# Optimization experiments

Hardware: AMD Instinct MI355X
Metric: run time of the kernel (lower is better)

## Reference

```python
import jax, jax.numpy as jnp
import numpy as np

B, N, D_IN, D_OUT = 512, 64, 2048, 1024
EPS = 1e-12  # layer_norm_epsilon


def setup_inputs() -> dict:
    key = jax.random.key(0)
    k0, k1, k2, k3, k4 = jax.random.split(key, 5)
    img_feats = jax.random.normal(k0, (B, N, D_IN), jnp.float32)
    boxes = jax.random.normal(k1, (B, N, 7), jnp.float32)
    box_mask = jax.random.randint(k2, (B, N), 0, 2, jnp.int32)
    obj_labels = jax.random.randint(k3, (B, N), 0, 91, jnp.int32)
    # Learned params: obj_downsample Linear(2048->1024), LayerNorm(1024)
    W = jax.random.normal(k4, (D_IN, D_OUT), jnp.float32) * 0.02
    b = jnp.zeros((D_OUT,), jnp.float32)
    ln_w = jnp.ones((D_OUT,), jnp.float32)
    ln_b = jnp.zeros((D_OUT,), jnp.float32)
    return {"img_feats": img_feats, "boxes": boxes, "box_mask": box_mask,
            "obj_labels": obj_labels, "W": W, "b": b, "ln_w": ln_w, "ln_b": ln_b}


def reference(img_feats, boxes, box_mask, obj_labels, W, b, ln_w, ln_b):
    # Dropout(p=0.1) is identity in eval mode.
    # Linear + ReLU applied to every (padded) box; per-row ops so padded rows
    # are computed then masked — same math as gathering valid rows first.
    h = jax.nn.relu(jnp.einsum('bnd,df->bnf', img_feats, W) + b)  # [B,N,1024]
    mu = jnp.mean(h, axis=-1, keepdims=True)
    var = jnp.mean(jnp.square(h - mu), axis=-1, keepdims=True)
    ln = (h - mu) * jax.lax.rsqrt(var + EPS) * ln_w + ln_b  # LayerNorm
    # pad_sequence repack: left-align each image's valid boxes (stable sort
    # keeps original order among valid boxes), zero the padded tail.
    order = jnp.argsort(1 - box_mask, axis=1, stable=True)  # valid first
    packed = jnp.take_along_axis(ln, order[:, :, None], axis=1)
    m = jnp.take_along_axis(box_mask, order, axis=1).astype(ln.dtype)
    return packed * m[:, :, None]  # obj_reps: [B, N, 1024]
```

## Files before the change

### kernel.cpp

```cpp
#include <hip/hip_runtime.h>
#include <hip/hip_bf16.h>

typedef __attribute__((ext_vector_type(8))) short short8;
typedef __attribute__((ext_vector_type(4))) short short4v;
typedef __attribute__((ext_vector_type(4))) float f32x4;

#define D_IN   2048
#define D_OUT  1024

__device__ __forceinline__ short f2bf(float x) {
    union { __hip_bfloat16 h; short s; } u;
    u.h = __float2bfloat16(x);
    return u.s;
}

__global__ void transpose_w_kernel(const float* __restrict__ W,
                                   short* __restrict__ Bt) {
    __shared__ float tile[32][33];
    int c0 = blockIdx.x * 32;
    int r0 = blockIdx.y * 32;
    int tc = threadIdx.x & 31;
    int tr = threadIdx.x >> 5;
#pragma unroll
    for (int i = 0; i < 32; i += 8)
        tile[tr + i][tc] = W[(long)(r0 + tr + i) * D_OUT + c0 + tc];
    __syncthreads();
#pragma unroll
    for (int i = 0; i < 32; i += 8)
        Bt[(long)(c0 + tr + i) * D_IN + r0 + tc] = f2bf(tile[tc][tr + i]);
}


#define BAR()    __builtin_amdgcn_s_barrier()
#define SB0()    __builtin_amdgcn_sched_barrier(0)
#define LGKM0()  do { asm volatile("s_waitcnt lgkmcnt(0)" ::: "memory"); SB0(); } while (0)
#define VMW(n)   do { asm volatile("s_waitcnt vmcnt(" #n ")" ::: "memory"); SB0(); } while (0)

__global__ __launch_bounds__(512, 2)
void fused_kernel(const float* __restrict__ img, const short* __restrict__ Bt,
                  const float* __restrict__ bias, const int* __restrict__ mask,
                  const float* __restrict__ lnw, const float* __restrict__ lnb,
                  float* __restrict__ out) {
    __shared__ char LDS[139264];
#define LDSB(buf) (LDS + (buf) * 65536)
#define LDSA(buf) (LDS + 131072 + (buf) * 4096)

    const int b    = blockIdx.x;
    const int tid  = threadIdx.x;
    const int lane = tid & 63;
    const int w    = tid >> 6;
    const int lrow = lane & 15;
    const int lchk = lane >> 4;

    const int  bsw   = (tid & 3) ^ ((tid >> 2) & 3) ^ ((tid >> 4) & 3);
    const short* bsrc0 = Bt + (long)(tid >> 2) * D_IN + bsw * 8;
    const long arowg = (long)b * 64 + (tid >> 3);
    const int  ak4   = (tid & 7) * 4;
    const int  arl    = tid >> 3;
    const int  achk   = (tid & 7) >> 1;
    const int  awoff  = (arl * 4 + (achk ^ (arl & 3) ^ ((arl >> 2) & 3))) * 16 + (tid & 1) * 8;
    const int  fsw = ((lchk ^ (lrow & 3) ^ ((lrow >> 2) & 3)) << 4);
    const int  afb = lrow * 64 + fsw;
    const int  bfb = w * 8192 + lrow * 64 + fsw;

#define B_GLD(buf, k0) do {                                                         \
    _Pragma("unroll") for (int i = 0; i < 8; ++i)                                   \
        __builtin_amdgcn_global_load_lds(                                           \
            (const __attribute__((address_space(1))) void*)(bsrc0 + (long)i * 128 * D_IN + (k0)), \
            (__attribute__((address_space(3))) void*)(LDSB(buf) + i * 8192 + tid * 16), 16, 0, 0); \
} while (0)
#define A_LOAD(k0)  do { stA = *(const float4*)(img + arowg * D_IN + (k0) + ak4); } while (0)
#define A_WRITE(buf) do {                                                           \
    short4v c_; c_[0] = f2bf(stA.x); c_[1] = f2bf(stA.y);                           \
    c_[2] = f2bf(stA.z); c_[3] = f2bf(stA.w);                                       \
    *(short4v*)(LDSA(buf) + awoff) = c_;                                            \
} while (0)
#define FRAG_READ(fa, fb, abuf, bbuf) do {                                          \
    _Pragma("unroll") for (int mi = 0; mi < 4; ++mi)                                \
        fa[mi] = *(const short8*)((abuf) + afb + mi * 1024);                        \
    _Pragma("unroll") for (int nf = 0; nf < 8; ++nf)                                \
        fb[nf] = *(const short8*)((bbuf) + bfb + nf * 1024);                        \
} while (0)
#define MFMA_T(fa, fb) do {                                                         \
    __builtin_amdgcn_s_setprio(1);                                                  \
    _Pragma("unroll") for (int mi = 0; mi < 4; ++mi)                                \
    _Pragma("unroll") for (int nf = 0; nf < 8; ++nf)                                \
        acc[mi][nf] = __builtin_amdgcn_mfma_f32_16x16x32_bf16(                      \
            fa[mi], fb[nf], acc[mi][nf], 0, 0, 0);                                  \
    __builtin_amdgcn_s_setprio(0);                                                  \
} while (0)
#define TILE(faP, fbP, faN, fbN, parbuf, npbuf, t) do {                             \
    VMW(0);                                    \
    A_WRITE(npbuf);                                              \
    LGKM0(); BAR(); SB0();                 \
    { int k2_ = (((t) + 2) & 63) * 32; A_LOAD(k2_); B_GLD(parbuf, k2_); }           \
    FRAG_READ(faN, fbN, LDSA(npbuf), LDSB(npbuf));                                  \
    MFMA_T(faP, fbP);                                                               \
} while (0)

    f32x4 acc[4][8];
#pragma unroll
    for (int i = 0; i < 4; ++i)
#pragma unroll
        for (int j = 0; j < 8; ++j) acc[i][j] = (f32x4)0.0f;

    float4 stA;
    short8 fA0[4], fB0[8], fA1[4], fB1[8];

    A_LOAD(0);
    B_GLD(0, 0);
    VMW(8);
    A_WRITE(0);
    A_LOAD(32);
    B_GLD(1, 32);
    VMW(9);
    LGKM0(); BAR(); SB0();
    FRAG_READ(fA0, fB0, LDSA(0), LDSB(0));

#pragma unroll 1
    for (int t = 0; t < 64; t += 2) {
        TILE(fA0, fB0, fA1, fB1, 0, 1, t);
        TILE(fA1, fB1, fA0, fB0, 1, 0, t + 1);
    }

    VMW(0); LGKM0(); BAR(); SB0();

    float* redS = (float*)LDS;
    float* redQ = (float*)(LDS + 2048);
    float* muT  = (float*)(LDS + 4096);
    float* rsT  = (float*)(LDS + 4352);

    float bb[8];
#pragma unroll
    for (int nf = 0; nf < 8; ++nf) bb[nf] = bias[w * 128 + nf * 16 + lrow];

    float s[4][4], q[4][4];
#pragma unroll
    for (int mi = 0; mi < 4; ++mi)
#pragma unroll
        for (int r = 0; r < 4; ++r) { s[mi][r] = 0.f; q[mi][r] = 0.f; }
#pragma unroll
    for (int mi = 0; mi < 4; ++mi)
#pragma unroll
        for (int nf = 0; nf < 8; ++nf)
#pragma unroll
            for (int r = 0; r < 4; ++r) {
                float v = fmaxf(acc[mi][nf][r] + bb[nf], 0.f);
                acc[mi][nf][r] = v;
                s[mi][r] += v;
                q[mi][r] += v * v;
            }
#pragma unroll
    for (int mi = 0; mi < 4; ++mi)
#pragma unroll
        for (int r = 0; r < 4; ++r)
#pragma unroll
            for (int off = 1; off <= 8; off <<= 1) {
                s[mi][r] += __shfl_xor(s[mi][r], off);
                q[mi][r] += __shfl_xor(q[mi][r], off);
            }
    if (lrow == 0) {
#pragma unroll
        for (int mi = 0; mi < 4; ++mi)
#pragma unroll
            for (int r = 0; r < 4; ++r) {
                int m = mi * 16 + lchk * 4 + r;
                redS[w * 64 + m] = s[mi][r];
                redQ[w * 64 + m] = q[mi][r];
            }
    }
    LGKM0(); BAR(); SB0();
    if (tid < 64) {
        float S = 0.f, Q = 0.f;
#pragma unroll
        for (int ww = 0; ww < 8; ++ww) { S += redS[ww * 64 + tid]; Q += redQ[ww * 64 + tid]; }
        float mu  = S * (1.0f / 1024.0f);
        float var = Q * (1.0f / 1024.0f) - mu * mu;
        muT[tid] = mu;
        rsT[tid] = rsqrtf(var + 1e-12f);
    }
    LGKM0(); BAR(); SB0();

    int mv = mask[(b << 6) | lane];
    unsigned long long bal = __ballot(mv != 0);
    int cnt = __popcll(bal);

    float lw[8], lb[8];
#pragma unroll
    for (int nf = 0; nf < 8; ++nf) {
        int col = w * 128 + nf * 16 + lrow;
        lw[nf] = lnw[col];
        lb[nf] = lnb[col];
    }
#pragma unroll
    for (int mi = 0; mi < 4; ++mi)
#pragma unroll
        for (int r = 0; r < 4; ++r) {
            int m = mi * 16 + lchk * 4 + r;
            if ((bal >> m) & 1ull) {
                int d = __popcll(bal & ((1ull << m) - 1ull));
                float mu = muT[m], rs = rsT[m];
                long obase = ((long)(b << 6) + d) * D_OUT + w * 128 + lrow;
#pragma unroll
                for (int nf = 0; nf < 8; ++nf)
                    out[obase + nf * 16] = (acc[mi][nf][r] - mu) * rs * lw[nf] + lb[nf];
            }
        }
    for (int d = cnt; d < 64; ++d) {
        float2 z = make_float2(0.f, 0.f);
        *(float2*)(out + ((long)(b << 6) + d) * D_OUT + w * 128 + lane * 2) = z;
    }
}

extern "C" void kernel_launch(void* const* d_in, const int* in_sizes, int n_in,
                              void* d_out, int out_size, void* d_ws, size_t ws_size,
                              hipStream_t stream) {
    const float* img  = (const float*)d_in[0];
    const int*   mask = (const int*)d_in[2];
    const float* W    = (const float*)d_in[4];
    const float* bias = (const float*)d_in[5];
    const float* lnw  = (const float*)d_in[6];
    const float* lnb  = (const float*)d_in[7];
    float* out = (float*)d_out;

    short* Bt = (short*)d_ws;

    transpose_w_kernel<<<dim3(D_OUT / 32, D_IN / 32), 256, 0, stream>>>(W, Bt);
    fused_kernel<<<512, 512, 0, stream>>>(img, Bt, bias, mask, lnw, lnb, out);
}
```

Before: 282.8 us.

## Replace double-buffered direct-to-LDS pipeline with single-buffer register-staged loads

Drops the two-stage LDS double buffer fed by global_load_lds and stages both the A and B tiles through registers, writing them into a single LDS buffer each iteration. This halves LDS use, from about 136KB to 68KB. Two barriers per k-step now separate the writes from the fragment reads, and the fragment reads no longer overlap the previous tile's MFMAs. The intent is simpler scheduling and possibly more resident blocks, at the cost of more VGPRs for the staged B data and less overlap between loads and compute.

```diff
diff --git a/kernel.cpp b/kernel.cpp
--- a/kernel.cpp
+++ b/kernel.cpp
@@ -34,16 +34,13 @@
 #define BAR()    __builtin_amdgcn_s_barrier()
 #define SB0()    __builtin_amdgcn_sched_barrier(0)
 #define LGKM0()  do { asm volatile("s_waitcnt lgkmcnt(0)" ::: "memory"); SB0(); } while (0)
-#define VMW(n)   do { asm volatile("s_waitcnt vmcnt(" #n ")" ::: "memory"); SB0(); } while (0)
 
 __global__ __launch_bounds__(512, 2)
 void fused_kernel(const float* __restrict__ img, const short* __restrict__ Bt,
                   const float* __restrict__ bias, const int* __restrict__ mask,
                   const float* __restrict__ lnw, const float* __restrict__ lnb,
                   float* __restrict__ out) {
-    __shared__ char LDS[139264];
-#define LDSB(buf) (LDS + (buf) * 65536)
-#define LDSA(buf) (LDS + 131072 + (buf) * 4096)
+    __shared__ char LDS[69632];
 
     const int b    = blockIdx.x;
     const int tid  = threadIdx.x;
@@ -52,51 +49,20 @@
     const int lrow = lane & 15;
     const int lchk = lane >> 4;
 
-    const int  bsw   = (tid & 3) ^ ((tid >> 2) & 3) ^ ((tid >> 4) & 3);
-    const short* bsrc0 = Bt + (long)(tid >> 2) * D_IN + bsw * 8;
-    const long arowg = (long)b * 64 + (tid >> 3);
-    const int  ak4   = (tid & 7) * 4;
-    const int  arl    = tid >> 3;
-    const int  achk   = (tid & 7) >> 1;
-    const int  awoff  = (arl * 4 + (achk ^ (arl & 3) ^ ((arl >> 2) & 3))) * 16 + (tid & 1) * 8;
-    const int  fsw = ((lchk ^ (lrow & 3) ^ ((lrow >> 2) & 3)) << 4);
-    const int  afb = lrow * 64 + fsw;
-    const int  bfb = w * 8192 + lrow * 64 + fsw;
-
-#define B_GLD(buf, k0) do {                                                         \
-    _Pragma("unroll") for (int i = 0; i < 8; ++i)                                   \
-        __builtin_amdgcn_global_load_lds(                                           \
-            (const __attribute__((address_space(1))) void*)(bsrc0 + (long)i * 128 * D_IN + (k0)), \
-            (__attribute__((address_space(3))) void*)(LDSB(buf) + i * 8192 + tid * 16), 16, 0, 0); \
-} while (0)
-#define A_LOAD(k0)  do { stA = *(const float4*)(img + arowg * D_IN + (k0) + ak4); } while (0)
-#define A_WRITE(buf) do {                                                           \
-    short4v c_; c_[0] = f2bf(stA.x); c_[1] = f2bf(stA.y);                           \
-    c_[2] = f2bf(stA.z); c_[3] = f2bf(stA.w);                                       \
-    *(short4v*)(LDSA(buf) + awoff) = c_;                                            \
-} while (0)
-#define FRAG_READ(fa, fb, abuf, bbuf) do {                                          \
-    _Pragma("unroll") for (int mi = 0; mi < 4; ++mi)                                \
-        fa[mi] = *(const short8*)((abuf) + afb + mi * 1024);                        \
-    _Pragma("unroll") for (int nf = 0; nf < 8; ++nf)                                \
-        fb[nf] = *(const short8*)((bbuf) + bfb + nf * 1024);                        \
-} while (0)
-#define MFMA_T(fa, fb) do {                                                         \
-    __builtin_amdgcn_s_setprio(1);                                                  \
-    _Pragma("unroll") for (int mi = 0; mi < 4; ++mi)                                \
-    _Pragma("unroll") for (int nf = 0; nf < 8; ++nf)                                \
-        acc[mi][nf] = __builtin_amdgcn_mfma_f32_16x16x32_bf16(                      \
-            fa[mi], fb[nf], acc[mi][nf], 0, 0, 0);                                  \
-    __builtin_amdgcn_s_setprio(0);                                                  \
-} while (0)
-#define TILE(faP, fbP, faN, fbN, parbuf, npbuf, t) do {                             \
-    VMW(0);                                    \
-    A_WRITE(npbuf);                                              \
-    LGKM0(); BAR(); SB0();                 \
-    { int k2_ = (((t) + 2) & 63) * 32; A_LOAD(k2_); B_GLD(parbuf, k2_); }           \
-    FRAG_READ(faN, fbN, LDSA(npbuf), LDSB(npbuf));                                  \
-    MFMA_T(faP, fbP);                                                               \
-} while (0)
+    const int brow = tid >> 2;
+    const int bchk = tid & 3;
+    const int bswz = bchk ^ (brow & 3) ^ ((tid >> 4) & 3);
+    const short* bsrc = Bt + (long)brow * D_IN + bchk * 8;
+    char* bdst = LDS + brow * 64 + bswz * 16;
+    const int arl   = tid >> 3;
+    const long arowg = (long)b * 64 + arl;
+    const int ak4   = (tid & 7) * 4;
+    const int achk  = (tid & 7) >> 1;
+    char* adst = LDS + 65536 + arl * 64
+               + ((achk ^ (arl & 3) ^ ((arl >> 2) & 3)) * 16) + (tid & 1) * 8;
+    const int fsw = ((lchk ^ (lrow & 3) ^ ((lrow >> 2) & 3)) << 4);
+    const char* afb = LDS + 65536 + lrow * 64 + fsw;
+    const char* bfb = LDS + w * 8192 + lrow * 64 + fsw;
 
     f32x4 acc[4][8];
 #pragma unroll
@@ -104,26 +70,53 @@
 #pragma unroll
         for (int j = 0; j < 8; ++j) acc[i][j] = (f32x4)0.0f;
 
+    short8 bst[8];
     float4 stA;
-    short8 fA0[4], fB0[8], fA1[4], fB1[8];
-
-    A_LOAD(0);
-    B_GLD(0, 0);
-    VMW(8);
-    A_WRITE(0);
-    A_LOAD(32);
-    B_GLD(1, 32);
-    VMW(9);
-    LGKM0(); BAR(); SB0();
-    FRAG_READ(fA0, fB0, LDSA(0), LDSB(0));
+    short8 fa[4], fb[8];
+
+    stA = *(const float4*)(img + arowg * D_IN + ak4);
+#pragma unroll
+    for (int j = 0; j < 8; ++j)
+        bst[j] = *(const short8*)(bsrc + (long)j * 128 * D_IN);
 
 #pragma unroll 1
-    for (int t = 0; t < 64; t += 2) {
-        TILE(fA0, fB0, fA1, fB1, 0, 1, t);
-        TILE(fA1, fB1, fA0, fB0, 1, 0, t + 1);
-    }
-
-    VMW(0); LGKM0(); BAR(); SB0();
+    for (int t = 0; t < 64; ++t) {
+        BAR(); SB0();
+        {
+            short4v ca;
+            ca[0] = f2bf(stA.x); ca[1] = f2bf(stA.y);
+            ca[2] = f2bf(stA.z); ca[3] = f2bf(stA.w);
+            *(short4v*)adst = ca;
+        }
+#pragma unroll
+        for (int j = 0; j < 8; ++j)
+            *(short8*)(bdst + j * 8192) = bst[j];
+        {
+            int k1 = ((t + 1) & 63) * 32;
+            stA = *(const float4*)(img + arowg * D_IN + k1 + ak4);
+#pragma unroll
+            for (int j = 0; j < 8; ++j)
+                bst[j] = *(const short8*)(bsrc + (long)j * 128 * D_IN + k1);
+        }
+        LGKM0();
+        BAR(); SB0();
+#pragma unroll
+        for (int mi = 0; mi < 4; ++mi)
+            fa[mi] = *(const short8*)(afb + mi * 1024);
+#pragma unroll
+        for (int nf = 0; nf < 8; ++nf)
+            fb[nf] = *(const short8*)(bfb + nf * 1024);
+        __builtin_amdgcn_s_setprio(1);
+#pragma unroll
+        for (int mi = 0; mi < 4; ++mi)
+#pragma unroll
+            for (int nf = 0; nf < 8; ++nf)
+                acc[mi][nf] = __builtin_amdgcn_mfma_f32_16x16x32_bf16(
+                    fa[mi], fb[nf], acc[mi][nf], 0, 0, 0);
+        __builtin_amdgcn_s_setprio(0);
+    }
+
+    __syncthreads();
 
     float* redS = (float*)LDS;
     float* redQ = (float*)(LDS + 2048);
@@ -169,7 +162,7 @@
                 redQ[w * 64 + m] = q[mi][r];
             }
     }
-    LGKM0(); BAR(); SB0();
+    __syncthreads();
     if (tid < 64) {
         float S = 0.f, Q = 0.f;
 #pragma unroll
@@ -179,7 +172,7 @@
         muT[tid] = mu;
         rsT[tid] = rsqrtf(var + 1e-12f);
     }
-    LGKM0(); BAR(); SB0();
+    __syncthreads();
 
     int mv = mask[(b << 6) | lane];
     unsigned long long bal = __ballot(mv != 0);
```

After: 281.3 us. No clear change (-0.5%).
